# Optimization experiments

Measured on AMD Instinct MI355X. Metric: run time of the kernel, lower is better.

Reference implementation:

```python
import jax, jax.numpy as jnp
import numpy as np

N = 100000
E = 3200000
F_IN = 128
H = 64
NUM_GRAPHS = 256


def setup_inputs() -> dict:
    key = jax.random.key(0)
    ks = jax.random.split(key, 8)
    x = jax.random.normal(ks[0], (N, F_IN), dtype=jnp.float32)
    edge_index = jax.random.randint(ks[1], (2, E), 0, N, dtype=jnp.int32)
    batch = jnp.sort(jax.random.randint(ks[2], (N,), 0, NUM_GRAPHS, dtype=jnp.int32))
    # Glorot-ish init for weights
    W1 = jax.random.normal(ks[3], (F_IN, H), dtype=jnp.float32) / np.sqrt(F_IN)
    b1 = jnp.zeros((H,), dtype=jnp.float32)
    W2 = jax.random.normal(ks[4], (H, H), dtype=jnp.float32) / np.sqrt(H)
    b2 = jnp.zeros((H,), dtype=jnp.float32)
    Wfc = jax.random.normal(ks[5], (H, 1), dtype=jnp.float32) / np.sqrt(H)
    bfc = jnp.zeros((1,), dtype=jnp.float32)
    return {"x": x, "edge_index": edge_index, "batch": batch,
            "W1": W1, "b1": b1, "W2": W2, "b2": b2, "Wfc": Wfc, "bfc": bfc}


def reference(x, edge_index, batch, W1, b1, W2, b2, Wfc, bfc):
    n = x.shape[0]
    loops = jnp.arange(n, dtype=edge_index.dtype)
    # GCN adds self-loops, then symmetric degree normalization
    src = jnp.concatenate([edge_index[0], loops])  # message sources
    dst = jnp.concatenate([edge_index[1], loops])  # message targets
    deg = jax.ops.segment_sum(jnp.ones_like(dst, dtype=x.dtype), dst, num_segments=n)
    d_inv_sqrt = jnp.where(deg > 0, jax.lax.rsqrt(deg), 0.0)
    norm = d_inv_sqrt[src] * d_inv_sqrt[dst]  # [E+N]

    def gcn_conv(h, W, b):
        hw = h @ W                                   # [N, H] small GEMM
        msg = hw[src] * norm[:, None]                # gather + scale  [E+N, H]
        agg = jax.ops.segment_sum(msg, dst, num_segments=n)  # scatter-add
        return agg + b

    h = jax.nn.relu(gcn_conv(x, W1, b1))
    h = jax.nn.relu(gcn_conv(h, W2, b2))

    # global_mean_pool over graphs in the batch
    pooled = jax.ops.segment_sum(h, batch, num_segments=NUM_GRAPHS)
    counts = jax.ops.segment_sum(jnp.ones((n,), dtype=h.dtype), batch, num_segments=NUM_GRAPHS)
    mean = pooled / jnp.maximum(counts, 1.0)[:, None]

    return mean @ Wfc + bfc  # [NUM_GRAPHS, 1]
```

## Files before the change

kernel.cpp:

```cpp
#include <hip/hip_runtime.h>

#define F_IN 128
#define HDIM 64
#define NUM_GRAPHS 256
#define SCAN_BLK 256
#define SCAN_CHUNK 2048

__global__ void hist_kernel(const int* __restrict__ dst, int* __restrict__ deg, int e) {
    int i = blockIdx.x * blockDim.x + threadIdx.x;
    if (i < e) atomicAdd(&deg[dst[i]], 1);
}

__global__ void scan_partial(const int* __restrict__ deg, int* __restrict__ partial, int n) {
    __shared__ int lds[SCAN_BLK];
    int b = blockIdx.x, t = threadIdx.x;
    int base = b * SCAN_CHUNK + t * 8;
    int s = 0;
#pragma unroll
    for (int j = 0; j < 8; ++j) { int idx = base + j; if (idx < n) s += deg[idx]; }
    lds[t] = s; __syncthreads();
    for (int off = SCAN_BLK / 2; off; off >>= 1) {
        if (t < off) lds[t] += lds[t + off];
        __syncthreads();
    }
    if (t == 0) partial[b] = lds[0];
}

__global__ void scan_spine(int* __restrict__ partial, int nb, int* __restrict__ off_end) {
    if (threadIdx.x == 0 && blockIdx.x == 0) {
        int run = 0;
        for (int i = 0; i < nb; ++i) { int v = partial[i]; partial[i] = run; run += v; }
        off_end[0] = run;
    }
}

__global__ void scan_final(const int* __restrict__ deg, const int* __restrict__ partial,
                           int* __restrict__ off, int* __restrict__ cursor,
                           float* __restrict__ dinv, int n) {
    __shared__ int lds[SCAN_BLK];
    int b = blockIdx.x, t = threadIdx.x;
    int base = b * SCAN_CHUNK + t * 8;
    int v[8]; int s = 0;
#pragma unroll
    for (int j = 0; j < 8; ++j) { int idx = base + j; v[j] = (idx < n) ? deg[idx] : 0; s += v[j]; }
    lds[t] = s; __syncthreads();
    for (int o = 1; o < SCAN_BLK; o <<= 1) {
        int y = (t >= o) ? lds[t - o] : 0;
        __syncthreads();
        if (t >= o) lds[t] += y;
        __syncthreads();
    }
    int run = partial[b] + lds[t] - s;
#pragma unroll
    for (int j = 0; j < 8; ++j) {
        int idx = base + j;
        if (idx < n) {
            off[idx] = run; cursor[idx] = run;
            dinv[idx] = rsqrtf((float)v[j] + 1.0f);
        }
        run += v[j];
    }
}

__global__ void fill_kernel(const int* __restrict__ src, const int* __restrict__ dst,
                            int* __restrict__ cursor, int* __restrict__ csr, int e) {
    int i = blockIdx.x * blockDim.x + threadIdx.x;
    if (i < e) {
        int pos = atomicAdd(&cursor[dst[i]], 1);
        csr[pos] = src[i];
    }
}

template<int K>
__global__ void gemm_kernel(const float* __restrict__ A, const float* __restrict__ W,
                            const float* __restrict__ dinv, float* __restrict__ out, int n) {
    __shared__ float Ws[K * 64];
    for (int i = threadIdx.x; i < K * 64; i += blockDim.x) Ws[i] = W[i];
    __syncthreads();
    int row  = blockIdx.x * (blockDim.x >> 6) + (threadIdx.x >> 6);
    int lane = threadIdx.x & 63;
    if (row >= n) return;
    const float4* ar = reinterpret_cast<const float4*>(A + (size_t)row * K);
    float acc = 0.f;
#pragma unroll
    for (int k4 = 0; k4 < K / 4; ++k4) {
        float4 av = ar[k4];
        acc = fmaf(av.x, Ws[(k4 * 4 + 0) * 64 + lane], acc);
        acc = fmaf(av.y, Ws[(k4 * 4 + 1) * 64 + lane], acc);
        acc = fmaf(av.z, Ws[(k4 * 4 + 2) * 64 + lane], acc);
        acc = fmaf(av.w, Ws[(k4 * 4 + 3) * 64 + lane], acc);
    }
    out[(size_t)row * 64 + lane] = acc * dinv[row];
}

template<bool POOL>
__global__ void gather_kernel(const int* __restrict__ off, const int* __restrict__ csr,
                              const float* __restrict__ hws, const float* __restrict__ dinv,
                              const float* __restrict__ b, const int* __restrict__ batch,
                              float* __restrict__ hout, float* __restrict__ pooled,
                              float* __restrict__ cnt, int n) {
    int d = blockIdx.x * (blockDim.x >> 6) + (threadIdx.x >> 6);
    int lane = threadIdx.x & 63;
    if (d >= n) return;
    int beg = off[d], end = off[d + 1];
    float acc0 = 0.f, acc1 = 0.f;
    int i = beg;
    for (; i + 2 <= end; i += 2) {
        int s0 = csr[i], s1 = csr[i + 1];
        acc0 += hws[(size_t)s0 * 64 + lane];
        acc1 += hws[(size_t)s1 * 64 + lane];
    }
    if (i < end) acc0 += hws[(size_t)csr[i] * 64 + lane];
    float v = (acc0 + acc1 + hws[(size_t)d * 64 + lane]) * dinv[d] + b[lane];
    v = fmaxf(v, 0.f);
    if (POOL) {
        int g = batch[d];
        atomicAdd(&pooled[(size_t)g * 64 + lane], v);
        if (lane == 0) atomicAdd(&cnt[g], 1.0f);
    } else {
        hout[(size_t)d * 64 + lane] = v;
    }
}

__global__ void final_kernel(const float* __restrict__ pooled, const float* __restrict__ cnt,
                             const float* __restrict__ Wfc, const float* __restrict__ bfc,
                             float* __restrict__ out) {
    int g = blockIdx.x;
    int lane = threadIdx.x;
    float c = fmaxf(cnt[g], 1.0f);
    float v = (pooled[(size_t)g * 64 + lane] / c) * Wfc[lane];
#pragma unroll
    for (int off = 32; off; off >>= 1) v += __shfl_down(v, off);
    if (lane == 0) out[g] = v + bfc[0];
}

extern "C" void kernel_launch(void* const* d_in, const int* in_sizes, int n_in,
                              void* d_out, int out_size, void* d_ws, size_t ws_size,
                              hipStream_t stream) {
    const float* x    = (const float*)d_in[0];
    const int*   ei   = (const int*)d_in[1];
    const int*   batch= (const int*)d_in[2];
    const float* W1   = (const float*)d_in[3];
    const float* b1   = (const float*)d_in[4];
    const float* W2   = (const float*)d_in[5];
    const float* b2   = (const float*)d_in[6];
    const float* Wfc  = (const float*)d_in[7];
    const float* bfc  = (const float*)d_in[8];
    float* out = (float*)d_out;

    const int n = in_sizes[0] / F_IN;
    const int e = in_sizes[1] / 2;
    const int* srcp = ei;
    const int* dstp = ei + e;

    size_t nAl = ((size_t)n + 256) & ~(size_t)255;
    int*   deg     = (int*)d_ws;
    int*   off     = deg + nAl;
    int*   cursor  = off + nAl;
    int*   partial = cursor + nAl;
    float* dinv    = (float*)(partial + 256);
    int*   csr     = (int*)(dinv + nAl);
    size_t eAl     = ((size_t)e + 255) & ~(size_t)255;
    float* hws     = (float*)(csr + eAl);
    float* h1      = hws + (size_t)n * 64;
    float* pooled  = h1 + (size_t)n * 64;
    float* cnt     = pooled + (size_t)NUM_GRAPHS * 64;

    const int nb = (n + SCAN_CHUNK - 1) / SCAN_CHUNK;

    hipMemsetAsync(deg, 0, (size_t)n * sizeof(int), stream);
    hist_kernel<<<(e + 255) / 256, 256, 0, stream>>>(dstp, deg, e);
    scan_partial<<<nb, SCAN_BLK, 0, stream>>>(deg, partial, n);
    scan_spine<<<1, 64, 0, stream>>>(partial, nb, &off[n]);
    scan_final<<<nb, SCAN_BLK, 0, stream>>>(deg, partial, off, cursor, dinv, n);
    fill_kernel<<<(e + 255) / 256, 256, 0, stream>>>(srcp, dstp, cursor, csr, e);

    gemm_kernel<F_IN><<<(n + 3) / 4, 256, 0, stream>>>(x, W1, dinv, hws, n);
    gather_kernel<false><<<(n + 3) / 4, 256, 0, stream>>>(off, csr, hws, dinv, b1, batch,
                                                          h1, nullptr, nullptr, n);

    gemm_kernel<HDIM><<<(n + 3) / 4, 256, 0, stream>>>(h1, W2, dinv, hws, n);
    hipMemsetAsync(pooled, 0, ((size_t)NUM_GRAPHS * 64 + NUM_GRAPHS) * sizeof(float), stream);
    gather_kernel<true><<<(n + 3) / 4, 256, 0, stream>>>(off, csr, hws, dinv, b2, batch,
                                                         nullptr, pooled, cnt, n);

    final_kernel<<<NUM_GRAPHS, 64, 0, stream>>>(pooled, cnt, Wfc, bfc, out);
}
```

Before: 1.545 ms.

## Process two destination nodes per wave with 8-way unrolled shuffle-broadcast gather

Each 64-lane wave now aggregates two destination nodes instead of one. Neighbor indices are loaded cooperatively, eight at a time, and broadcast with shuffles. Up to sixteen independent row gathers are then kept in flight with separate accumulators, raising memory-level parallelism in the latency-bound CSR gather. The cost is more registers per thread, half as many waves, and tail handling that issues redundant loads for partial groups.

```diff
diff --git a/kernel.cpp b/kernel.cpp
--- a/kernel.cpp
+++ b/kernel.cpp
@@ -99,26 +99,93 @@
                               const float* __restrict__ b, const int* __restrict__ batch,
                               float* __restrict__ hout, float* __restrict__ pooled,
                               float* __restrict__ cnt, int n) {
-    int d = blockIdx.x * (blockDim.x >> 6) + (threadIdx.x >> 6);
+    int w = blockIdx.x * (blockDim.x >> 6) + (threadIdx.x >> 6);
     int lane = threadIdx.x & 63;
-    if (d >= n) return;
-    int beg = off[d], end = off[d + 1];
-    float acc0 = 0.f, acc1 = 0.f;
-    int i = beg;
-    for (; i + 2 <= end; i += 2) {
-        int s0 = csr[i], s1 = csr[i + 1];
-        acc0 += hws[(size_t)s0 * 64 + lane];
-        acc1 += hws[(size_t)s1 * 64 + lane];
-    }
-    if (i < end) acc0 += hws[(size_t)csr[i] * 64 + lane];
-    float v = (acc0 + acc1 + hws[(size_t)d * 64 + lane]) * dinv[d] + b[lane];
+    int d0 = 2 * w, d1 = 2 * w + 1;
+    if (d0 >= n) return;
+    bool has1 = (d1 < n);
+    int i0 = off[d0], e0 = off[d0 + 1];
+    int i1 = has1 ? off[d1] : 0, e1 = has1 ? off[d1 + 1] : 0;
+    int l8 = lane & 7;
+
+    float acc0[8], acc1[8];
+#pragma unroll
+    for (int j = 0; j < 8; ++j) { acc0[j] = 0.f; acc1[j] = 0.f; }
+
+    while (i0 + 8 <= e0 && i1 + 8 <= e1) {
+        int v0 = csr[i0 + l8];
+        int v1 = csr[i1 + l8];
+#pragma unroll
+        for (int j = 0; j < 8; ++j) {
+            int s0 = __shfl(v0, j);
+            acc0[j] += hws[(size_t)s0 * 64 + lane];
+            int s1 = __shfl(v1, j);
+            acc1[j] += hws[(size_t)s1 * 64 + lane];
+        }
+        i0 += 8; i1 += 8;
+    }
+    while (i0 + 8 <= e0) {
+        int v0 = csr[i0 + l8];
+#pragma unroll
+        for (int j = 0; j < 8; ++j) {
+            int s0 = __shfl(v0, j);
+            acc0[j] += hws[(size_t)s0 * 64 + lane];
+        }
+        i0 += 8;
+    }
+    while (i1 + 8 <= e1) {
+        int v1 = csr[i1 + l8];
+#pragma unroll
+        for (int j = 0; j < 8; ++j) {
+            int s1 = __shfl(v1, j);
+            acc1[j] += hws[(size_t)s1 * 64 + lane];
+        }
+        i1 += 8;
+    }
+    int m0 = e0 - i0;
+    if (m0 > 0) {
+        int v0 = csr[(i0 + l8 < e0) ? (i0 + l8) : (e0 - 1)];
+#pragma unroll
+        for (int j = 0; j < 7; ++j) {
+            int s0 = __shfl(v0, j);
+            float f = hws[(size_t)s0 * 64 + lane];
+            if (j < m0) acc0[j] += f;
+        }
+    }
+    int m1 = e1 - i1;
+    if (m1 > 0) {
+        int v1 = csr[(i1 + l8 < e1) ? (i1 + l8) : (e1 - 1)];
+#pragma unroll
+        for (int j = 0; j < 7; ++j) {
+            int s1 = __shfl(v1, j);
+            float f = hws[(size_t)s1 * 64 + lane];
+            if (j < m1) acc1[j] += f;
+        }
+    }
+
+    float t0 = ((acc0[0] + acc0[1]) + (acc0[2] + acc0[3])) +
+               ((acc0[4] + acc0[5]) + (acc0[6] + acc0[7]));
+    float v = (t0 + hws[(size_t)d0 * 64 + lane]) * dinv[d0] + b[lane];
     v = fmaxf(v, 0.f);
     if (POOL) {
-        int g = batch[d];
+        int g = batch[d0];
         atomicAdd(&pooled[(size_t)g * 64 + lane], v);
         if (lane == 0) atomicAdd(&cnt[g], 1.0f);
     } else {
-        hout[(size_t)d * 64 + lane] = v;
+        hout[(size_t)d0 * 64 + lane] = v;
+    }
+    if (has1) {
+        float t1 = ((acc1[0] + acc1[1]) + (acc1[2] + acc1[3])) +
+                   ((acc1[4] + acc1[5]) + (acc1[6] + acc1[7]));
+        float v1v = (t1 + hws[(size_t)d1 * 64 + lane]) * dinv[d1] + b[lane];
+        v1v = fmaxf(v1v, 0.f);
+        if (POOL) {
+            int g = batch[d1];
+            atomicAdd(&pooled[(size_t)g * 64 + lane], v1v);
+            if (lane == 0) atomicAdd(&cnt[g], 1.0f);
+        } else {
+            hout[(size_t)d1 * 64 + lane] = v1v;
+        }
     }
 }
 
@@ -167,6 +234,8 @@
     float* cnt     = pooled + (size_t)NUM_GRAPHS * 64;
 
     const int nb = (n + SCAN_CHUNK - 1) / SCAN_CHUNK;
+    const int nwave = (n + 1) / 2;
+    const int gblocks = (nwave + 3) / 4;
 
     hipMemsetAsync(deg, 0, (size_t)n * sizeof(int), stream);
     hist_kernel<<<(e + 255) / 256, 256, 0, stream>>>(dstp, deg, e);
@@ -176,13 +245,13 @@
     fill_kernel<<<(e + 255) / 256, 256, 0, stream>>>(srcp, dstp, cursor, csr, e);
 
     gemm_kernel<F_IN><<<(n + 3) / 4, 256, 0, stream>>>(x, W1, dinv, hws, n);
-    gather_kernel<false><<<(n + 3) / 4, 256, 0, stream>>>(off, csr, hws, dinv, b1, batch,
-                                                          h1, nullptr, nullptr, n);
+    gather_kernel<false><<<gblocks, 256, 0, stream>>>(off, csr, hws, dinv, b1, batch,
+                                                      h1, nullptr, nullptr, n);
 
     gemm_kernel<HDIM><<<(n + 3) / 4, 256, 0, stream>>>(h1, W2, dinv, hws, n);
     hipMemsetAsync(pooled, 0, ((size_t)NUM_GRAPHS * 64 + NUM_GRAPHS) * sizeof(float), stream);
-    gather_kernel<true><<<(n + 3) / 4, 256, 0, stream>>>(off, csr, hws, dinv, b2, batch,
-                                                         nullptr, pooled, cnt, n);
+    gather_kernel<true><<<gblocks, 256, 0, stream>>>(off, csr, hws, dinv, b2, batch,
+                                                     nullptr, pooled, cnt, n);
 
     final_kernel<<<NUM_GRAPHS, 64, 0, stream>>>(pooled, cnt, Wfc, bfc, out);
 }
```

Measured after the change: 1.349 ms. 12.7% less time.
